# Optimization experiments

Hardware: AMD Instinct MI355X
Metric: run time of the kernel (lower is better)

## Reference

```python
import jax, jax.numpy as jnp
import numpy as np

EPS = 1e-6

def _rmsnorm(x, w):
    return x * jax.lax.rsqrt(jnp.mean(x * x, axis=-1, keepdims=True) + EPS) * w

def _short_conv_silu(x, w):
    # x: [B,T,C], w: [C,K] depthwise causal conv then SiLU
    K = w.shape[1]
    T = x.shape[1]
    xp = jnp.pad(x, ((0, 0), (K - 1, 0), (0, 0)))
    y = sum(xp[:, i:i + T, :] * w[:, i] for i in range(K))
    return jax.nn.silu(y)

def _l2norm(x):
    return x * jax.lax.rsqrt(jnp.sum(x * x, axis=-1, keepdims=True) + EPS)

def setup_inputs():
    key = jax.random.key(0)
    ks = jax.random.split(key, 20)
    B, T, D = 4, 2048, 1024
    H, dk, dv = 8, 96, 192
    KD, VD, I = H * dk, H * dv, 4096
    s = 0.02
    r = lambda k, shp: jax.random.normal(k, shp, jnp.float32) * s
    return {
        "x": jax.random.normal(ks[0], (B, T, D), jnp.float32),
        "Wq": r(ks[1], (D, KD)),
        "Wk": r(ks[2], (D, KD)),
        "Wv": r(ks[3], (D, VD)),
        "Wb": r(ks[4], (D, H)),
        "Wa": r(ks[5], (D, H)),
        "A_log": jnp.log(jax.random.uniform(ks[6], (H,), jnp.float32, 1.0, 16.0)),
        "dt_bias": jax.random.normal(ks[7], (H,), jnp.float32) * 0.1,
        "conv_q_w": jax.random.normal(ks[8], (KD, 4), jnp.float32) * 0.2,
        "conv_k_w": jax.random.normal(ks[9], (KD, 4), jnp.float32) * 0.2,
        "conv_v_w": jax.random.normal(ks[10], (VD, 4), jnp.float32) * 0.2,
        "Wg": r(ks[11], (D, VD)),
        "onorm_w": jnp.ones((dv,), jnp.float32),
        "Wo": r(ks[12], (VD, D)),
        "norm1_w": jnp.ones((D,), jnp.float32),
        "norm2_w": jnp.ones((D,), jnp.float32),
        "Wgate": r(ks[13], (D, I)),
        "Wup": r(ks[14], (D, I)),
        "Wdown": r(ks[15], (I, D)),
    }

def reference(x, Wq, Wk, Wv, Wb, Wa, A_log, dt_bias, conv_q_w, conv_k_w, conv_v_w,
              Wg, onorm_w, Wo, norm1_w, norm2_w, Wgate, Wup, Wdown):
    B, T, D = x.shape
    H = A_log.shape[0]
    dk = Wq.shape[1] // H
    dv = Wv.shape[1] // H
    scale = dk ** -0.5

    # --- pre-norm + token mixer (GatedDeltaNet attention) ---
    h = _rmsnorm(x, norm1_w)
    q = _short_conv_silu(h @ Wq, conv_q_w).reshape(B, T, H, dk)
    k = _short_conv_silu(h @ Wk, conv_k_w).reshape(B, T, H, dk)
    v = _short_conv_silu(h @ Wv, conv_v_w).reshape(B, T, H, dv)
    q = _l2norm(q) * scale
    k = _l2norm(k)
    beta = jax.nn.sigmoid(h @ Wb)                               # [B,T,H]
    g = -jnp.exp(A_log) * jax.nn.softplus(h @ Wa + dt_bias)    # [B,T,H], <= 0

    # gated delta-rule recurrence: S_t = exp(g_t)*S_{t-1} + k_t (beta_t*(v_t - S^T k_t))^T
    def step(S, inp):
        q_t, k_t, v_t, g_t, b_t = inp
        S = S * jnp.exp(g_t)[..., None, None]
        v_old = jnp.einsum('bhk,bhkv->bhv', k_t, S)
        delta = (v_t - v_old) * b_t[..., None]
        S = S + jnp.einsum('bhk,bhv->bhkv', k_t, delta)
        o_t = jnp.einsum('bhk,bhkv->bhv', q_t, S)
        return S, o_t

    S0 = jnp.zeros((B, H, dk, dv), x.dtype)
    xs = (jnp.moveaxis(q, 1, 0), jnp.moveaxis(k, 1, 0), jnp.moveaxis(v, 1, 0),
          jnp.moveaxis(g, 1, 0), jnp.moveaxis(beta, 1, 0))
    _, o = jax.lax.scan(step, S0, xs)
    o = jnp.moveaxis(o, 0, 1)                                   # [B,T,H,dv]

    # gated RMSNorm output gate, then output projection
    g_out = (h @ Wg).reshape(B, T, H, dv)
    o = _rmsnorm(o, onorm_w) * jax.nn.silu(g_out)
    x = x + o.reshape(B, T, H * dv) @ Wo

    # --- pre-norm + SwiGLU MLP ---
    h2 = _rmsnorm(x, norm2_w)
    mlp = (jax.nn.silu(h2 @ Wgate) * (h2 @ Wup)) @ Wdown
    return x + mlp
```

## Files before the change

kernel.cpp:

```cpp
#include <hip/hip_runtime.h>
#include <hip/hip_bf16.h>

typedef __hip_bfloat16 bf16;
typedef unsigned short us;
typedef short short8v __attribute__((ext_vector_type(8)));
typedef float f32x4 __attribute__((ext_vector_type(4)));
typedef __attribute__((address_space(3))) unsigned int lds_u32;
typedef __attribute__((address_space(1))) const unsigned int glb_u32;

#define GLOAD16(gp, lp) __builtin_amdgcn_global_load_lds((glb_u32*)(gp), (lds_u32*)(lp), 16, 0, 0)

#define Bz 4
#define Tz 2048
#define Dz 1024
#define Hz 8
#define DKz 96
#define DVz 192
#define KDz 768
#define VDz 1536
#define Iz 4096
#define BTz (Bz*Tz)

static __device__ __forceinline__ float us2f(us s){
  return __uint_as_float(((unsigned)s) << 16);
}
static __device__ __forceinline__ us f2bs(float f){
  bf16 t = __float2bfloat16(f);
  return *(us*)&t;
}
static __device__ __forceinline__ float sigmoidf_(float x){ return 1.f/(1.f+expf(-x)); }
static __device__ __forceinline__ float siluf_(float x){ return x*sigmoidf_(x); }

#define DPPADD(x, ctrl) \
  ((x) + __int_as_float(__builtin_amdgcn_update_dpp(0, __float_as_int(x), (ctrl), 0xF, 0xF, true)))
static __device__ __forceinline__ float gsum16(float x){
  x = DPPADD(x, 0xB1);
  x = DPPADD(x, 0x4E);
  x = DPPADD(x, 0x141);
  x = DPPADD(x, 0x140);
  return x;
}

__global__ __launch_bounds__(256) void wprep_kernel(
    const float* __restrict__ Wsrc, us* __restrict__ WTdst, int K, int N)
{
  __shared__ float t[32][33];
  const int k0 = blockIdx.x*32, n0 = blockIdx.y*32;
  const int c = threadIdx.x & 31, r8 = threadIdx.x >> 5;
  #pragma unroll
  for (int i=0;i<4;i++){
    const int r = r8 + i*8;
    t[r][c] = Wsrc[(size_t)(k0+r)*N + n0 + c];
  }
  __syncthreads();
  #pragma unroll
  for (int i=0;i<4;i++){
    const int r = r8 + i*8;
    WTdst[(size_t)(n0+r)*K + k0 + c] = f2bs(t[c][r]);
  }
}

__global__ __launch_bounds__(256) void rmsnorm_kernel(
    const float* __restrict__ x, const float* __restrict__ w, bf16* __restrict__ out)
{
  const int row = blockIdx.x;
  const float* xr = x + (size_t)row*Dz;
  const int i0 = threadIdx.x*4;
  float4 xv = *(const float4*)(xr + i0);
  float ss = xv.x*xv.x+xv.y*xv.y+xv.z*xv.z+xv.w*xv.w;
  #pragma unroll
  for (int off=32; off>=1; off>>=1) ss += __shfl_xor(ss, off);
  __shared__ float red[4];
  if ((threadIdx.x&63)==0) red[threadIdx.x>>6] = ss;
  __syncthreads();
  ss = red[0]+red[1]+red[2]+red[3];
  const float inv = rsqrtf(ss*(1.f/Dz) + 1e-6f);
  float4 wv = *(const float4*)(w + i0);
  ushort4 ov;
  ov.x=f2bs(xv.x*inv*wv.x); ov.y=f2bs(xv.y*inv*wv.y);
  ov.z=f2bs(xv.z*inv*wv.z); ov.w=f2bs(xv.w*inv*wv.w);
  *(ushort4*)((us*)out + (size_t)row*Dz + i0) = ov;
}

template<int MODE>
__global__ __launch_bounds__(256, 2) void mgemm_kernel(
    const bf16* __restrict__ A, const us* __restrict__ BT,
    const void* __restrict__ res, void* __restrict__ Cout,
    int M, int N, int K)
{
  __shared__ us As[128*64];
  __shared__ us Bs[128*64];
  const int nwgx = gridDim.x;
  const int lid = blockIdx.y*nwgx + blockIdx.x;
  const int cpx = (nwgx*gridDim.y) >> 3;
  const int swz = (lid & 7)*cpx + (lid >> 3);
  const int m0 = (swz / nwgx)*128, n0 = (swz % nwgx)*128;
  const int tid = threadIdx.x;
  const int wid = tid >> 6, lane = tid & 63;
  const int wr = wid >> 1, wc = wid & 1;
  const int fq = lane >> 4, fr = lane & 15;

  const us* Ab = (const us*)A + (size_t)(m0 + (tid>>3))*K + (tid&7)*8;
  const us* Bb = BT + (size_t)(n0 + (tid>>3))*K + (tid&7)*8;
  char* AsB = (char*)As;
  char* BsB = (char*)Bs;
  const int ldsoff = wid*1024;

  f32x4 acc[4][4] = {};
  const int nk = K >> 6;
  for (int kt = 0; kt < nk; ++kt){
    const int kb = kt*64;
    #pragma unroll
    for (int i=0;i<4;i++){
      GLOAD16(Ab + (size_t)(32*i)*K + kb, AsB + ldsoff + i*4096);
      GLOAD16(Bb + (size_t)(32*i)*K + kb, BsB + ldsoff + i*4096);
    }
    __syncthreads();
    #pragma unroll
    for (int ks=0; ks<2; ks++){
      short8v af[4], bf[4];
      #pragma unroll
      for (int r=0;r<4;r++)
        af[r] = *(const short8v*)&As[(wr*64 + r*16 + fr)*64 + ks*32 + fq*8];
      #pragma unroll
      for (int c=0;c<4;c++)
        bf[c] = *(const short8v*)&Bs[(wc*64 + c*16 + fr)*64 + ks*32 + fq*8];
      #pragma unroll
      for (int r=0;r<4;r++)
        #pragma unroll
        for (int c=0;c<4;c++)
          acc[r][c] = __builtin_amdgcn_mfma_f32_16x16x32_bf16(af[r], bf[c], acc[r][c], 0, 0, 0);
    }
    __syncthreads();
  }
  #pragma unroll
  for (int r=0;r<4;r++){
    #pragma unroll
    for (int c=0;c<4;c++){
      const int col = n0 + wc*64 + c*16 + fr;
      #pragma unroll
      for (int jj=0;jj<4;jj++){
        const int row = m0 + wr*64 + r*16 + fq*4 + jj;
        const size_t idx = (size_t)row*N + col;
        const float a = acc[r][c][jj];
        if (MODE==0){
          ((us*)Cout)[idx] = f2bs(a);
        } else {
          ((float*)Cout)[idx] = a + ((const float*)res)[idx];
        }
      }
    }
  }
}

__global__ __launch_bounds__(256, 2) void proj_gemm_kernel(
    const bf16* __restrict__ A, const us* __restrict__ BT,
    us* __restrict__ preq, us* __restrict__ prek,
    us* __restrict__ prev, us* __restrict__ gout,
    int M, int N, int K)
{
  __shared__ us As[128*64];
  __shared__ us Bs[128*64];
  const int nwgx = gridDim.x;
  const int lid = blockIdx.y*nwgx + blockIdx.x;
  const int cpx = (nwgx*gridDim.y) >> 3;
  const int swz = (lid & 7)*cpx + (lid >> 3);
  const int m0 = (swz / nwgx)*128, n0 = (swz % nwgx)*128;
  const int tid = threadIdx.x;
  const int wid = tid >> 6, lane = tid & 63;
  const int wr = wid >> 1, wc = wid & 1;
  const int fq = lane >> 4, fr = lane & 15;

  const us* Ab = (const us*)A + (size_t)(m0 + (tid>>3))*K + (tid&7)*8;
  const us* Bb = BT + (size_t)(n0 + (tid>>3))*K + (tid&7)*8;
  char* AsB = (char*)As;
  char* BsB = (char*)Bs;
  const int ldsoff = wid*1024;

  f32x4 acc[4][4] = {};
  const int nk = K >> 6;
  for (int kt = 0; kt < nk; ++kt){
    const int kb = kt*64;
    #pragma unroll
    for (int i=0;i<4;i++){
      GLOAD16(Ab + (size_t)(32*i)*K + kb, AsB + ldsoff + i*4096);
      GLOAD16(Bb + (size_t)(32*i)*K + kb, BsB + ldsoff + i*4096);
    }
    __syncthreads();
    #pragma unroll
    for (int ks=0; ks<2; ks++){
      short8v af[4], bf[4];
      #pragma unroll
      for (int r=0;r<4;r++)
        af[r] = *(const short8v*)&As[(wr*64 + r*16 + fr)*64 + ks*32 + fq*8];
      #pragma unroll
      for (int c=0;c<4;c++)
        bf[c] = *(const short8v*)&Bs[(wc*64 + c*16 + fr)*64 + ks*32 + fq*8];
      #pragma unroll
      for (int r=0;r<4;r++)
        #pragma unroll
        for (int c=0;c<4;c++)
          acc[r][c] = __builtin_amdgcn_mfma_f32_16x16x32_bf16(af[r], bf[c], acc[r][c], 0, 0, 0);
    }
    __syncthreads();
  }
  us* dst; int col0, Nout;
  if (n0 < 768)      { dst = preq; col0 = n0;        Nout = 768;  }
  else if (n0 < 1536){ dst = prek; col0 = n0 - 768;  Nout = 768;  }
  else if (n0 < 3072){ dst = prev; col0 = n0 - 1536; Nout = 1536; }
  else               { dst = gout; col0 = n0 - 3072; Nout = 1536; }
  #pragma unroll
  for (int r=0;r<4;r++){
    #pragma unroll
    for (int c=0;c<4;c++){
      const int col = col0 + wc*64 + c*16 + fr;
      #pragma unroll
      for (int jj=0;jj<4;jj++){
        const int row = m0 + wr*64 + r*16 + fq*4 + jj;
        dst[(size_t)row*Nout + col] = f2bs(acc[r][c][jj]);
      }
    }
  }
}

__global__ __launch_bounds__(256, 2) void mgemm_dual_kernel(
    const bf16* __restrict__ A, const us* __restrict__ BT1, const us* __restrict__ BT2,
    us* __restrict__ Cout, int M, int N, int K)
{
  __shared__ us As[128*64];
  __shared__ us Bs1[128*64];
  __shared__ us Bs2[128*64];
  const int nwgx = gridDim.x;
  const int lid = blockIdx.y*nwgx + blockIdx.x;
  const int cpx = (nwgx*gridDim.y) >> 3;
  const int swz = (lid & 7)*cpx + (lid >> 3);
  const int m0 = (swz / nwgx)*128, n0 = (swz % nwgx)*128;
  const int tid = threadIdx.x;
  const int wid = tid >> 6, lane = tid & 63;
  const int wr = wid >> 1, wc = wid & 1;
  const int fq = lane >> 4, fr = lane & 15;

  const us* Ab  = (const us*)A + (size_t)(m0 + (tid>>3))*K + (tid&7)*8;
  const us* Bb1 = BT1 + (size_t)(n0 + (tid>>3))*K + (tid&7)*8;
  const us* Bb2 = BT2 + (size_t)(n0 + (tid>>3))*K + (tid&7)*8;
  char* AsB  = (char*)As;
  char* BsB1 = (char*)Bs1;
  char* BsB2 = (char*)Bs2;
  const int ldsoff = wid*1024;

  f32x4 acc1[4][4] = {};
  f32x4 acc2[4][4] = {};
  const int nk = K >> 6;
  for (int kt = 0; kt < nk; ++kt){
    const int kb = kt*64;
    #pragma unroll
    for (int i=0;i<4;i++){
      GLOAD16(Ab  + (size_t)(32*i)*K + kb, AsB  + ldsoff + i*4096);
      GLOAD16(Bb1 + (size_t)(32*i)*K + kb, BsB1 + ldsoff + i*4096);
      GLOAD16(Bb2 + (size_t)(32*i)*K + kb, BsB2 + ldsoff + i*4096);
    }
    __syncthreads();
    #pragma unroll
    for (int ks=0; ks<2; ks++){
      short8v af[4], bf1[4], bf2[4];
      #pragma unroll
      for (int r=0;r<4;r++)
        af[r] = *(const short8v*)&As[(wr*64 + r*16 + fr)*64 + ks*32 + fq*8];
      #pragma unroll
      for (int c=0;c<4;c++){
        bf1[c] = *(const short8v*)&Bs1[(wc*64 + c*16 + fr)*64 + ks*32 + fq*8];
        bf2[c] = *(const short8v*)&Bs2[(wc*64 + c*16 + fr)*64 + ks*32 + fq*8];
      }
      #pragma unroll
      for (int r=0;r<4;r++)
        #pragma unroll
        for (int c=0;c<4;c++){
          acc1[r][c] = __builtin_amdgcn_mfma_f32_16x16x32_bf16(af[r], bf1[c], acc1[r][c], 0, 0, 0);
          acc2[r][c] = __builtin_amdgcn_mfma_f32_16x16x32_bf16(af[r], bf2[c], acc2[r][c], 0, 0, 0);
        }
    }
    __syncthreads();
  }
  #pragma unroll
  for (int r=0;r<4;r++){
    #pragma unroll
    for (int c=0;c<4;c++){
      const int col = n0 + wc*64 + c*16 + fr;
      #pragma unroll
      for (int jj=0;jj<4;jj++){
        const int row = m0 + wr*64 + r*16 + fq*4 + jj;
        Cout[(size_t)row*N + col] = f2bs(siluf_(acc1[r][c][jj]) * acc2[r][c][jj]);
      }
    }
  }
}

__global__ __launch_bounds__(256) void beta_g_kernel(
    const bf16* __restrict__ hh, const float* __restrict__ Wb, const float* __restrict__ Wa,
    const float* __restrict__ A_log, const float* __restrict__ dt_bias,
    float2* __restrict__ meta)
{
  const int row = blockIdx.x;
  const us* hr = (const us*)hh + (size_t)row*Dz;
  float ab[8]={0,0,0,0,0,0,0,0}, aa[8]={0,0,0,0,0,0,0,0};
  for (int kk=threadIdx.x; kk<Dz; kk+=256){
    const float hv = us2f(hr[kk]);
    float4 b0 = *(const float4*)(Wb + kk*8);
    float4 b1 = *(const float4*)(Wb + kk*8 + 4);
    float4 a0 = *(const float4*)(Wa + kk*8);
    float4 a1 = *(const float4*)(Wa + kk*8 + 4);
    ab[0]=fmaf(hv,b0.x,ab[0]); ab[1]=fmaf(hv,b0.y,ab[1]);
    ab[2]=fmaf(hv,b0.z,ab[2]); ab[3]=fmaf(hv,b0.w,ab[3]);
    ab[4]=fmaf(hv,b1.x,ab[4]); ab[5]=fmaf(hv,b1.y,ab[5]);
    ab[6]=fmaf(hv,b1.z,ab[6]); ab[7]=fmaf(hv,b1.w,ab[7]);
    aa[0]=fmaf(hv,a0.x,aa[0]); aa[1]=fmaf(hv,a0.y,aa[1]);
    aa[2]=fmaf(hv,a0.z,aa[2]); aa[3]=fmaf(hv,a0.w,aa[3]);
    aa[4]=fmaf(hv,a1.x,aa[4]); aa[5]=fmaf(hv,a1.y,aa[5]);
    aa[6]=fmaf(hv,a1.z,aa[6]); aa[7]=fmaf(hv,a1.w,aa[7]);
  }
  #pragma unroll
  for (int off=32; off>=1; off>>=1){
    #pragma unroll
    for (int n=0;n<8;n++){ ab[n]+=__shfl_xor(ab[n],off); aa[n]+=__shfl_xor(aa[n],off); }
  }
  __shared__ float red[4][16];
  const int wv = threadIdx.x>>6, ln = threadIdx.x&63;
  if (ln==0){
    #pragma unroll
    for (int n=0;n<8;n++){ red[wv][n]=ab[n]; red[wv][8+n]=aa[n]; }
  }
  __syncthreads();
  if (threadIdx.x < 8){
    const int n = threadIdx.x;
    float sb = red[0][n]+red[1][n]+red[2][n]+red[3][n];
    float sa = red[0][8+n]+red[1][8+n]+red[2][8+n]+red[3][8+n];
    float xx = sa + dt_bias[n];
    float sp = (xx > 20.f) ? xx : log1pf(expf(xx));
    float eg = expf(-expf(A_log[n])*sp);
    float bt = 1.f/(1.f+expf(-sb));
    meta[(size_t)row*Hz + n] = make_float2(eg, bt);
  }
}

__global__ __launch_bounds__(64) void conv_kq_kernel(
    const bf16* __restrict__ preq, const bf16* __restrict__ prek,
    const float* __restrict__ wqc, const float* __restrict__ wkc,
    us* __restrict__ kqn)
{
  const int idx = blockIdx.x; const int h = idx & 7; const int bt = idx >> 3;
  const int t = bt & (Tz-1);
  const int lane = threadIdx.x;
  const us* Q = (const us*)preq;
  const us* K = (const us*)prek;
  const int c0 = h*DKz + lane, c1 = c0 + 64;
  const bool hi = lane < 32;
  float yq0=0.f, yq1=0.f, yk0=0.f, yk1=0.f;
  #pragma unroll
  for (int i=0;i<4;i++){
    const int ti = t - 3 + i;
    if (ti >= 0){
      const size_t rowb = (size_t)(bt-3+i)*KDz;
      yq0 = fmaf(us2f(Q[rowb + c0]), wqc[c0*4+i], yq0);
      yk0 = fmaf(us2f(K[rowb + c0]), wkc[c0*4+i], yk0);
      if (hi){
        yq1 = fmaf(us2f(Q[rowb + c1]), wqc[c1*4+i], yq1);
        yk1 = fmaf(us2f(K[rowb + c1]), wkc[c1*4+i], yk1);
      }
    }
  }
  yq0 = siluf_(yq0); yk0 = siluf_(yk0);
  yq1 = hi ? siluf_(yq1) : 0.f;
  yk1 = hi ? siluf_(yk1) : 0.f;
  float ssq = yq0*yq0 + yq1*yq1;
  float ssk = yk0*yk0 + yk1*yk1;
  #pragma unroll
  for (int off=32; off>=1; off>>=1){ ssq += __shfl_xor(ssq,off); ssk += __shfl_xor(ssk,off); }
  const float iq = rsqrtf(ssq + 1e-6f) * 0.10206207262f;
  const float ik = rsqrtf(ssk + 1e-6f);
  const size_t base = (size_t)bt*1536 + (size_t)h*192;
  kqn[base + lane]      = f2bs(yk0*ik);
  kqn[base + 96 + lane] = f2bs(yq0*iq);
  if (hi){
    kqn[base + 64 + lane]      = f2bs(yk1*ik);
    kqn[base + 96 + 64 + lane] = f2bs(yq1*iq);
  }
}

__global__ __launch_bounds__(256) void conv_apply_v_kernel(
    const bf16* __restrict__ prev, const float* __restrict__ wvc, bf16* __restrict__ vn)
{
  const int bt = blockIdx.y; const int ccol = blockIdx.x*256 + threadIdx.x;
  const int t = bt & (Tz-1);
  const us* X = (const us*)prev;
  float acc = 0.f;
  #pragma unroll
  for (int i=0;i<4;i++){
    const int ti = t - 3 + i;
    if (ti >= 0) acc = fmaf(us2f(X[(size_t)(bt-3+i)*VDz + ccol]), wvc[ccol*4+i], acc);
  }
  ((us*)vn)[(size_t)bt*VDz + ccol] = f2bs(siluf_(acc));
}

__global__ __launch_bounds__(192, 1) void scan_kernel(
    const us* __restrict__ kqn, const bf16* __restrict__ vn,
    const float2* __restrict__ meta, bf16* __restrict__ o)
{
  const int blk = blockIdx.x;
  const int bh = blk >> 4, sp = blk & 15;
  const int b = bh >> 3, h = bh & 7;
  const int tid = threadIdx.x;
  const int g = tid & 15;
  const int j = tid >> 4;
  const int vc = h*DVz + sp*12 + j;

  __shared__ float kq[2][8][192];

  const us* KQ = kqn + (size_t)b*Tz*1536 + h*192 + tid;
  const us* VP = (const us*)vn + (size_t)b*Tz*VDz + vc;
  us* op = (us*)o + (size_t)b*Tz*VDz + vc;
  const float2* MP = meta + (size_t)b*Tz*Hz + h;

  float S[6];
  #pragma unroll
  for (int m=0;m<6;m++) S[m]=0.f;

  float ced[8], egb[8], cvb[8];

  #pragma unroll
  for (int s=0;s<8;s++){
    kq[0][s][tid] = us2f(KQ[(size_t)s*1536]);
    const float cv = us2f(VP[(size_t)s*VDz]);
    const float2 m = MP[(size_t)s*Hz];
    ced[s] = m.x; egb[s] = m.x*m.y; cvb[s] = cv*m.y;
  }
  __syncthreads();

  for (int ph=0; ph<Tz/8; ph++){
    const int base = ph*8;
    const int p = ph & 1;
    const bool more = (base + 8 < Tz);
    const int nb = more ? base + 8 : base;
    float nkq[8], nv[8]; float2 nm[8];
    #pragma unroll
    for (int s=0;s<8;s++){
      nkq[s] = us2f(KQ[(size_t)(nb+s)*1536]);
      nv[s]  = us2f(VP[(size_t)(nb+s)*VDz]);
      nm[s]  = MP[(size_t)(nb+s)*Hz];
    }
    float2 kf[2][3], qf[2][3];
    #pragma unroll
    for (int m=0;m<3;m++){
      kf[0][m] = *(const float2*)&kq[p][0][g*6 + m*2];
      qf[0][m] = *(const float2*)&kq[p][0][96 + g*6 + m*2];
    }
    #pragma unroll
    for (int s=0;s<8;s++){
      const int cu = s & 1, nx = cu ^ 1;
      if (s < 7){
        #pragma unroll
        for (int m=0;m<3;m++){
          kf[nx][m] = *(const float2*)&kq[p][s+1][g*6 + m*2];
          qf[nx][m] = *(const float2*)&kq[p][s+1][96 + g*6 + m*2];
        }
      }
      float a0, a1;
      a0 = kf[cu][0].x*S[0];          a1 = kf[cu][0].y*S[1];
      a0 = fmaf(kf[cu][1].x,S[2],a0); a1 = fmaf(kf[cu][1].y,S[3],a1);
      a0 = fmaf(kf[cu][2].x,S[4],a0); a1 = fmaf(kf[cu][2].y,S[5],a1);
      const float pv = gsum16(a0+a1);
      const float eg = ced[s];
      const float delta = fmaf(-egb[s], pv, cvb[s]);
      float o0, o1, t0;
      t0 = fmaf(eg,S[0], kf[cu][0].x*delta); S[0]=t0; o0 = qf[cu][0].x*t0;
      t0 = fmaf(eg,S[1], kf[cu][0].y*delta); S[1]=t0; o1 = qf[cu][0].y*t0;
      t0 = fmaf(eg,S[2], kf[cu][1].x*delta); S[2]=t0; o0 = fmaf(qf[cu][1].x,t0,o0);
      t0 = fmaf(eg,S[3], kf[cu][1].y*delta); S[3]=t0; o1 = fmaf(qf[cu][1].y,t0,o1);
      t0 = fmaf(eg,S[4], kf[cu][2].x*delta); S[4]=t0; o0 = fmaf(qf[cu][2].x,t0,o0);
      t0 = fmaf(eg,S[5], kf[cu][2].y*delta); S[5]=t0; o1 = fmaf(qf[cu][2].y,t0,o1);
      const float po = gsum16(o0+o1);
      if (g == 0) op[(size_t)(base+s)*VDz] = f2bs(po);
    }
    if (more){
      #pragma unroll
      for (int s=0;s<8;s++){
        kq[p^1][s][tid] = nkq[s];
        ced[s] = nm[s].x; egb[s] = nm[s].x*nm[s].y; cvb[s] = nv[s]*nm[s].y;
      }
    }
    __syncthreads();
  }
}

__global__ __launch_bounds__(64) void gate_out_kernel(
    const bf16* __restrict__ o, const bf16* __restrict__ gout,
    const float* __restrict__ onw, bf16* __restrict__ og)
{
  const size_t base = (size_t)blockIdx.x * DVz;
  const int lane = threadIdx.x;
  const us* O = (const us*)o;
  float x0 = us2f(O[base+lane]), x1 = us2f(O[base+64+lane]), x2 = us2f(O[base+128+lane]);
  float ss = x0*x0 + x1*x1 + x2*x2;
  #pragma unroll
  for (int off=32; off>=1; off>>=1) ss += __shfl_xor(ss, off);
  const float inv = rsqrtf(ss*(1.f/DVz) + 1e-6f);
  const us* G = (const us*)gout;
  us* OG = (us*)og;
  float xs[3] = {x0, x1, x2};
  #pragma unroll
  for (int i=0;i<3;i++){
    const int c = lane + 64*i;
    const float gv = us2f(G[base+c]);
    OG[base+c] = f2bs(xs[i]*inv*onw[c] * siluf_(gv));
  }
}

extern "C" void kernel_launch(void* const* d_in, const int* in_sizes, int n_in,
                              void* d_out, int out_size, void* d_ws, size_t ws_size,
                              hipStream_t stream) {
  const float* x        = (const float*)d_in[0];
  const float* Wq       = (const float*)d_in[1];
  const float* Wk       = (const float*)d_in[2];
  const float* Wv       = (const float*)d_in[3];
  const float* Wb       = (const float*)d_in[4];
  const float* Wa       = (const float*)d_in[5];
  const float* A_log    = (const float*)d_in[6];
  const float* dt_bias  = (const float*)d_in[7];
  const float* conv_q_w = (const float*)d_in[8];
  const float* conv_k_w = (const float*)d_in[9];
  const float* conv_v_w = (const float*)d_in[10];
  const float* Wg       = (const float*)d_in[11];
  const float* onorm_w  = (const float*)d_in[12];
  const float* Wo       = (const float*)d_in[13];
  const float* norm1_w  = (const float*)d_in[14];
  const float* norm2_w  = (const float*)d_in[15];
  const float* Wgate    = (const float*)d_in[16];
  const float* Wup      = (const float*)d_in[17];
  const float* Wdown    = (const float*)d_in[18];

  char* W = (char*)d_ws;
  us* WoT    = (us*)(W + 0);
  us* WgateT = (us*)(W + 3145728);
  us* WupT   = (us*)(W + 11534336);
  us* WdownT = (us*)(W + 19922944);
  us* WqkvgT = (us*)(W + 28311552);
  bf16*   h_   = (bf16*)  (W + 37748736);
  bf16*   preq = (bf16*)  (W + 54525952);
  bf16*   prek = (bf16*)  (W + 67108864);
  bf16*   prev = (bf16*)  (W + 79691776);
  float2* meta = (float2*)(W + 104857600);
  bf16*   gout = (bf16*)  (W + 105906176);
  us*    kqn   = (us*)   (W + 28311552);
  bf16*  vn    = (bf16*) (W + 54525952);
  bf16*  o_    = (bf16*) (W + 79691776);
  float* x2    = (float*)(W + 79691776);
  bf16*  og    = (bf16*) (W + 28311552);
  bf16*  h2    = (bf16*) (W + 113246208);
  bf16*  gateC = (bf16*) (W + 28311552);

  wprep_kernel<<<dim3(48,32),  256, 0, stream>>>(Wo,    WoT,    1536, 1024);
  wprep_kernel<<<dim3(32,128), 256, 0, stream>>>(Wgate, WgateT, 1024, 4096);
  wprep_kernel<<<dim3(32,128), 256, 0, stream>>>(Wup,   WupT,   1024, 4096);
  wprep_kernel<<<dim3(128,32), 256, 0, stream>>>(Wdown, WdownT, 4096, 1024);
  wprep_kernel<<<dim3(32,24),  256, 0, stream>>>(Wq,    WqkvgT,             1024, 768);
  wprep_kernel<<<dim3(32,24),  256, 0, stream>>>(Wk,    WqkvgT +  768*1024, 1024, 768);
  wprep_kernel<<<dim3(32,48),  256, 0, stream>>>(Wv,    WqkvgT + 1536*1024, 1024, 1536);
  wprep_kernel<<<dim3(32,48),  256, 0, stream>>>(Wg,    WqkvgT + 3072*1024, 1024, 1536);
  rmsnorm_kernel<<<BTz, 256, 0, stream>>>(x, norm1_w, h_);
  proj_gemm_kernel<<<dim3(36,64), 256, 0, stream>>>(h_, WqkvgT,
      (us*)preq, (us*)prek, (us*)prev, (us*)gout, BTz, 4608, Dz);
  beta_g_kernel<<<BTz, 256, 0, stream>>>(h_, Wb, Wa, A_log, dt_bias, meta);
  conv_kq_kernel<<<BTz*Hz, 64, 0, stream>>>(preq, prek, conv_q_w, conv_k_w, kqn);
  conv_apply_v_kernel<<<dim3(6, BTz), 256, 0, stream>>>(prev, conv_v_w, vn);
  scan_kernel<<<Bz*Hz*16, 192, 0, stream>>>(kqn, vn, meta, o_);
  gate_out_kernel<<<BTz*Hz, 64, 0, stream>>>(o_, gout, onorm_w, og);
  mgemm_kernel<1><<<dim3(8,64), 256, 0, stream>>>(og, WoT, x, x2, BTz, Dz, VDz);
  rmsnorm_kernel<<<BTz, 256, 0, stream>>>(x2, norm2_w, h2);
  for (int c = 0; c < 2; c++){
    const bf16*  h2c = h2 + (size_t)c*4096*Dz;
    const float* x2c = x2 + (size_t)c*4096*Dz;
    float*       out = (float*)d_out + (size_t)c*4096*Dz;
    mgemm_dual_kernel<<<dim3(32,32), 256, 0, stream>>>(h2c, WgateT, WupT, (us*)gateC,
                                                       4096, Iz, Dz);
    mgemm_kernel<1><<<dim3(8,32),  256, 0, stream>>>(gateC, WdownT, x2c, out, 4096, Dz, Iz);
  }
}
```

Baseline: 1.152 ms.

## Merge weight-prep launches into one kernel and double scan chunk size

The eight per-matrix weight transpose/convert launches become one kernel that maps a flat block index to a segment and tile. This is meant to cut launch overhead and the tail gaps between small launches. Separately, the scan kernel now processes 16 timesteps per phase instead of 8, halving the barriers and prefetch rounds per sequence. The cost is more registers and shared memory per scan block.

```diff
diff --git a/kernel.cpp b/kernel.cpp
--- a/kernel.cpp
+++ b/kernel.cpp
@@ -41,22 +41,41 @@
   return x;
 }
 
-__global__ __launch_bounds__(256) void wprep_kernel(
-    const float* __restrict__ Wsrc, us* __restrict__ WTdst, int K, int N)
-{
+__global__ __launch_bounds__(256) void wprep_all_kernel(
+    const float* __restrict__ s0, const float* __restrict__ s1,
+    const float* __restrict__ s2, const float* __restrict__ s3,
+    const float* __restrict__ s4, const float* __restrict__ s5,
+    const float* __restrict__ s6, const float* __restrict__ s7,
+    us* __restrict__ d0, us* __restrict__ d1, us* __restrict__ d2,
+    us* __restrict__ d3, us* __restrict__ d4, us* __restrict__ d5,
+    us* __restrict__ d6, us* __restrict__ d7)
+{
+  const int NT[8] = {1536,4096,4096,4096,768,768,1536,1536};
+  const int KS[8] = {1536,1024,1024,4096,1024,1024,1024,1024};
+  const int NS[8] = {1024,4096,4096,1024,768,768,1536,1536};
+  int b = blockIdx.x, seg = 0;
+  #pragma unroll
+  for (int i=0;i<7;i++){ if (b >= NT[seg]){ b -= NT[seg]; seg++; } }
+  const float* src = seg==0?s0: seg==1?s1: seg==2?s2: seg==3?s3:
+                     seg==4?s4: seg==5?s5: seg==6?s6: s7;
+  us* dst = seg==0?d0: seg==1?d1: seg==2?d2: seg==3?d3:
+            seg==4?d4: seg==5?d5: seg==6?d6: d7;
+  const int K = KS[seg], N = NS[seg];
+  const int ktiles = K >> 5;
+  const int k0 = (b % ktiles)*32, n0 = (b / ktiles)*32;
+
   __shared__ float t[32][33];
-  const int k0 = blockIdx.x*32, n0 = blockIdx.y*32;
   const int c = threadIdx.x & 31, r8 = threadIdx.x >> 5;
   #pragma unroll
   for (int i=0;i<4;i++){
     const int r = r8 + i*8;
-    t[r][c] = Wsrc[(size_t)(k0+r)*N + n0 + c];
+    t[r][c] = src[(size_t)(k0+r)*N + n0 + c];
   }
   __syncthreads();
   #pragma unroll
   for (int i=0;i<4;i++){
     const int r = r8 + i*8;
-    WTdst[(size_t)(n0+r)*K + k0 + c] = f2bs(t[c][r]);
+    dst[(size_t)(n0+r)*K + k0 + c] = f2bs(t[c][r]);
   }
 }
 
@@ -413,7 +432,7 @@
   const int j = tid >> 4;
   const int vc = h*DVz + sp*12 + j;
 
-  __shared__ float kq[2][8][192];
+  __shared__ float kq[2][16][192];
 
   const us* KQ = kqn + (size_t)b*Tz*1536 + h*192 + tid;
   const us* VP = (const us*)vn + (size_t)b*Tz*VDz + vc;
@@ -424,10 +443,10 @@
   #pragma unroll
   for (int m=0;m<6;m++) S[m]=0.f;
 
-  float ced[8], egb[8], cvb[8];
-
-  #pragma unroll
-  for (int s=0;s<8;s++){
+  float ced[16], egb[16], cvb[16];
+
+  #pragma unroll
+  for (int s=0;s<16;s++){
     kq[0][s][tid] = us2f(KQ[(size_t)s*1536]);
     const float cv = us2f(VP[(size_t)s*VDz]);
     const float2 m = MP[(size_t)s*Hz];
@@ -435,14 +454,14 @@
   }
   __syncthreads();
 
-  for (int ph=0; ph<Tz/8; ph++){
-    const int base = ph*8;
+  for (int ph=0; ph<Tz/16; ph++){
+    const int base = ph*16;
     const int p = ph & 1;
-    const bool more = (base + 8 < Tz);
-    const int nb = more ? base + 8 : base;
-    float nkq[8], nv[8]; float2 nm[8];
-    #pragma unroll
-    for (int s=0;s<8;s++){
+    const bool more = (base + 16 < Tz);
+    const int nb = more ? base + 16 : base;
+    float nkq[16], nv[16]; float2 nm[16];
+    #pragma unroll
+    for (int s=0;s<16;s++){
       nkq[s] = us2f(KQ[(size_t)(nb+s)*1536]);
       nv[s]  = us2f(VP[(size_t)(nb+s)*VDz]);
       nm[s]  = MP[(size_t)(nb+s)*Hz];
@@ -454,9 +473,9 @@
       qf[0][m] = *(const float2*)&kq[p][0][96 + g*6 + m*2];
     }
     #pragma unroll
-    for (int s=0;s<8;s++){
+    for (int s=0;s<16;s++){
       const int cu = s & 1, nx = cu ^ 1;
-      if (s < 7){
+      if (s < 15){
         #pragma unroll
         for (int m=0;m<3;m++){
           kf[nx][m] = *(const float2*)&kq[p][s+1][g*6 + m*2];
@@ -482,7 +501,7 @@
     }
     if (more){
       #pragma unroll
-      for (int s=0;s<8;s++){
+      for (int s=0;s<16;s++){
         kq[p^1][s][tid] = nkq[s];
         ced[s] = nm[s].x; egb[s] = nm[s].x*nm[s].y; cvb[s] = nv[s]*nm[s].y;
       }
@@ -557,14 +576,10 @@
   bf16*  h2    = (bf16*) (W + 113246208);
   bf16*  gateC = (bf16*) (W + 28311552);
 
-  wprep_kernel<<<dim3(48,32),  256, 0, stream>>>(Wo,    WoT,    1536, 1024);
-  wprep_kernel<<<dim3(32,128), 256, 0, stream>>>(Wgate, WgateT, 1024, 4096);
-  wprep_kernel<<<dim3(32,128), 256, 0, stream>>>(Wup,   WupT,   1024, 4096);
-  wprep_kernel<<<dim3(128,32), 256, 0, stream>>>(Wdown, WdownT, 4096, 1024);
-  wprep_kernel<<<dim3(32,24),  256, 0, stream>>>(Wq,    WqkvgT,             1024, 768);
-  wprep_kernel<<<dim3(32,24),  256, 0, stream>>>(Wk,    WqkvgT +  768*1024, 1024, 768);
-  wprep_kernel<<<dim3(32,48),  256, 0, stream>>>(Wv,    WqkvgT + 1536*1024, 1024, 1536);
-  wprep_kernel<<<dim3(32,48),  256, 0, stream>>>(Wg,    WqkvgT + 3072*1024, 1024, 1536);
+  wprep_all_kernel<<<18432, 256, 0, stream>>>(
+      Wo, Wgate, Wup, Wdown, Wq, Wk, Wv, Wg,
+      WoT, WgateT, WupT, WdownT,
+      WqkvgT, WqkvgT + 768*1024, WqkvgT + 1536*1024, WqkvgT + 3072*1024);
   rmsnorm_kernel<<<BTz, 256, 0, stream>>>(x, norm1_w, h_);
   proj_gemm_kernel<<<dim3(36,64), 256, 0, stream>>>(h_, WqkvgT,
       (us*)preq, (us*)prek, (us*)prev, (us*)gout, BTz, 4608, Dz);
```

Measured after the change: 1.133 ms. Within noise of the previous version (-1.7%).
